# Optimization experiments

Measured on AMD Instinct MI355X. Metric: run time of the kernel, lower is better.

Reference implementation:

```python
import jax, jax.numpy as jnp
import numpy as np

EPS = 1e-12  # torch F.normalize eps

def _normalize(x):
    n = jnp.sqrt(jnp.sum(x * x, axis=-1, keepdims=True))
    return x / jnp.maximum(n, EPS)

def bgs_extended(d6s):
    # d6s: [B, N, D, 3, 2] -> rotation [B, N, D, 3, 3] (columns b1,b2,b3)
    b1 = _normalize(d6s[..., :, 0])
    a2 = d6s[..., :, 1]
    dot = jnp.sum(b1 * a2, axis=-1, keepdims=True)
    b2 = _normalize(a2 - dot * b1)
    b3 = jnp.cross(b1, b2, axis=-1)
    return jnp.stack([b1, b2, b3], axis=-1)

def setup_inputs() -> dict:
    key = jax.random.key(0)
    k1, k2, k3, k4, k5 = jax.random.split(key, 5)
    B, N, D, F = 8, 8192, 64, 64
    X = jax.random.normal(k1, (B, N, D, 3), dtype=jnp.float32)
    J = jax.random.normal(k2, (B, N, D, 3, 2), dtype=jnp.float32)
    A = jax.random.normal(k3, (F, D), dtype=jnp.float32)
    Bm = jax.random.normal(k4, (F, D), dtype=jnp.float32)
    C = jax.random.normal(k5, (F, D), dtype=jnp.float32)
    return {"X": X, "J": J, "A": A, "Bm": Bm, "C": C}

def reference(X, J, A, Bm, C):
    R = bgs_extended(J)  # [B,N,D,3,3]
    # RT_i X = dot(column i of R, X) -> compute all three at once: [B,N,D,3]
    RTX = jnp.einsum('bndki,bndk->bndi', R, X)
    rt0, rt1, rt2 = RTX[..., 0:1], RTX[..., 1:2], RTX[..., 2:3]
    # get_rrtx(i, R, s) == R[..., :, i] * s
    a_term = R[..., :, 0] * rt0 + R[..., :, 1] * rt1
    b_term = R[..., :, 1] * rt0 - R[..., :, 0] * rt1
    c_term = R[..., :, 2] * rt2
    Y = (jnp.einsum('fe,bnei->bnfi', A, a_term)
         + jnp.einsum('fe,bnei->bnfi', Bm, b_term)
         + jnp.einsum('fe,bnei->bnfi', C, c_term))
    return Y
```

## Files before the change

### kernel.cpp

```cpp
#include <hip/hip_runtime.h>

typedef __bf16 bf16;
typedef bf16 bf16x8 __attribute__((ext_vector_type(8)));
typedef float f32x4 __attribute__((ext_vector_type(4)));
typedef unsigned int u32;

#define PTS 16
#define WREG 4800

__device__ __forceinline__ void gld_lds16(const void* g, void* l) {
    __builtin_amdgcn_global_load_lds(
        (const __attribute__((address_space(1))) u32*)g,
        (__attribute__((address_space(3))) u32*)l, 16, 0, 0);
}

__global__ __launch_bounds__(256, 7)
void affine_linear_fused(const float* __restrict__ X, const float* __restrict__ J,
                         const float* __restrict__ A, const float* __restrict__ Bm,
                         const float* __restrict__ C, float* __restrict__ Y)
{
    __shared__ __attribute__((aligned(128))) unsigned char lds[4 * WREG];

    const int tid  = threadIdx.x;
    const int wave = tid >> 6;
    const int lane = tid & 63;
    const int l16  = lane & 15;
    const int lq   = lane >> 4;
    const long bn0 = (long)blockIdx.x * PTS;

    unsigned char* wbase = &lds[wave * WREG];

    const float* xg = X + (bn0 + wave * 4) * 192;
    #pragma unroll
    for (int t = 0; t < 3; ++t)
        gld_lds16(xg + t * 256 + lane * 4, wbase + t * 1024);

    const float* jg = J + (bn0 + wave * 4) * 384 + lane * 6;
    float jv[4][6];
    #pragma unroll
    for (int q = 0; q < 4; ++q) {
        float2 ja = *(const float2*)(jg + q * 384 + 0);
        float2 jb = *(const float2*)(jg + q * 384 + 2);
        float2 jc = *(const float2*)(jg + q * 384 + 4);
        jv[q][0] = ja.x; jv[q][1] = ja.y;
        jv[q][2] = jb.x; jv[q][3] = jb.y;
        jv[q][4] = jc.x; jv[q][5] = jc.y;
    }

    __asm__ volatile("s_waitcnt vmcnt(0)" ::: "memory");

    const float* xlds = (const float*)wbase;
    float xv[4][3];
    #pragma unroll
    for (int q = 0; q < 4; ++q) {
        const float* xp = xlds + q * 192 + lane * 3;
        xv[q][0] = xp[0]; xv[q][1] = xp[1]; xv[q][2] = xp[2];
    }

    #pragma unroll
    for (int q = 0; q < 4; ++q) {
        float a1x = jv[q][0], a2x = jv[q][1];
        float a1y = jv[q][2], a2y = jv[q][3];
        float a1z = jv[q][4], a2z = jv[q][5];
        float xx = xv[q][0], xy = xv[q][1], xz = xv[q][2];

        float n1sq = a1x*a1x + a1y*a1y + a1z*a1z;
        float inv1 = __builtin_amdgcn_rsqf(fmaxf(n1sq, 1e-24f));
        float b1x = a1x*inv1, b1y = a1y*inv1, b1z = a1z*inv1;
        float dot = b1x*a2x + b1y*a2y + b1z*a2z;
        float ux = a2x - dot*b1x, uy = a2y - dot*b1y, uz = a2z - dot*b1z;
        float n2sq = ux*ux + uy*uy + uz*uz;
        float inv2 = __builtin_amdgcn_rsqf(fmaxf(n2sq, 1e-24f));
        float b2x = ux*inv2, b2y = uy*inv2, b2z = uz*inv2;
        float b3x = b1y*b2z - b1z*b2y;
        float b3y = b1z*b2x - b1x*b2z;
        float b3z = b1x*b2y - b1y*b2x;

        float rt0 = b1x*xx + b1y*xy + b1z*xz;
        float rt1 = b2x*xx + b2y*xy + b2z*xz;
        float rt2 = b3x*xx + b3y*xy + b3z*xz;

        float at0 = b1x*rt0 + b2x*rt1;
        float at1 = b1y*rt0 + b2y*rt1;
        float at2 = b1z*rt0 + b2z*rt1;
        float bt0 = b2x*rt0 - b1x*rt1;
        float bt1 = b2y*rt0 - b1y*rt1;
        float bt2 = b2z*rt0 - b1z*rt1;
        float ct0 = b3x*rt2, ct1 = b3y*rt2, ct2 = b3z*rt2;

        bf16* r0 = (bf16*)(wbase + (q*3 + 0) * 400);
        bf16* r1 = (bf16*)(wbase + (q*3 + 1) * 400);
        bf16* r2 = (bf16*)(wbase + (q*3 + 2) * 400);
        r0[lane] = (bf16)at0; r0[64+lane] = (bf16)bt0; r0[128+lane] = (bf16)ct0;
        r1[lane] = (bf16)at1; r1[64+lane] = (bf16)bt1; r1[128+lane] = (bf16)ct1;
        r2[lane] = (bf16)at2; r2[64+lane] = (bf16)bt2; r2[128+lane] = (bf16)ct2;
    }

    const int f = wave * 16 + l16;
    const float* wp0 = A + f * 64 + lq * 8;
    f32x4 wlo = *(const f32x4*)wp0;
    f32x4 whi = *(const f32x4*)(wp0 + 4);

    __syncthreads();

    const unsigned char* arow[3];
    #pragma unroll
    for (int mt = 0; mt < 3; ++mt) {
        int m  = mt * 16 + l16;
        int wv = m / 12;
        int r  = m - wv * 12;
        arow[mt] = &lds[wv * WREG + r * 400] + lq * 16;
    }
    f32x4 acc[3];
    #pragma unroll
    for (int mt = 0; mt < 3; ++mt) acc[mt] = (f32x4){0.f, 0.f, 0.f, 0.f};

    #pragma unroll
    for (int kk = 0; kk < 6; ++kk) {
        f32x4 nlo = wlo, nhi = whi;
        if (kk < 5) {
            const float* src = (kk + 1 < 2) ? A : (kk + 1 < 4) ? Bm : C;
            const float* p = src + f * 64 + ((kk + 1) & 1) * 32 + lq * 8;
            nlo = *(const f32x4*)p;
            nhi = *(const f32x4*)(p + 4);
        }
        bf16x8 w;
        w[0] = (bf16)wlo[0]; w[1] = (bf16)wlo[1]; w[2] = (bf16)wlo[2]; w[3] = (bf16)wlo[3];
        w[4] = (bf16)whi[0]; w[5] = (bf16)whi[1]; w[6] = (bf16)whi[2]; w[7] = (bf16)whi[3];
        #pragma unroll
        for (int mt = 0; mt < 3; ++mt) {
            bf16x8 af = *(const bf16x8*)(arow[mt] + kk * 64);
            acc[mt] = __builtin_amdgcn_mfma_f32_16x16x32_bf16(af, w, acc[mt], 0, 0, 0);
        }
        wlo = nlo; whi = nhi;
    }

    __syncthreads();

    float* yw = (float*)wbase;
    #pragma unroll
    for (int mt = 0; mt < 3; ++mt) {
        #pragma unroll
        for (int r = 0; r < 4; ++r) {
            int m  = mt * 16 + lq * 4 + r;
            int wv = m / 12;
            int rr = m - wv * 12;
            int q  = rr / 3;
            int i  = rr - q * 3;
            int p  = wv * 4 + q;
            yw[p * 48 + l16 * 3 + i] = acc[mt][r];
        }
    }

    const f32x4* ysrc = (const f32x4*)yw;
    #pragma unroll
    for (int v = 0; v < 3; ++v) {
        int vi = v * 64 + lane;
        int p  = vi / 12;
        int vo = vi - p * 12;
        f32x4* dst = (f32x4*)(Y + (bn0 + p) * 192 + wave * 48) + vo;
        *dst = ysrc[vi];
    }
}

extern "C" void kernel_launch(void* const* d_in, const int* in_sizes, int n_in,
                              void* d_out, int out_size, void* d_ws, size_t ws_size,
                              hipStream_t stream) {
    const float* X  = (const float*)d_in[0];
    const float* J  = (const float*)d_in[1];
    const float* A  = (const float*)d_in[2];
    const float* Bm = (const float*)d_in[3];
    const float* C  = (const float*)d_in[4];
    float* Y = (float*)d_out;

    const int points = in_sizes[0] / (64 * 3);
    const int blocks = points / PTS;
    affine_linear_fused<<<blocks, 256, 0, stream>>>(X, J, A, Bm, C, Y);
}
```

Before: 206.9 us.

## Process four point groups per block with register prefetch and hoisted bf16 weights

```diff
diff --git a/kernel.cpp b/kernel.cpp
--- a/kernel.cpp
+++ b/kernel.cpp
@@ -3,18 +3,35 @@
 typedef __bf16 bf16;
 typedef bf16 bf16x8 __attribute__((ext_vector_type(8)));
 typedef float f32x4 __attribute__((ext_vector_type(4)));
-typedef unsigned int u32;
 
 #define PTS 16
+#define NG 4
 #define WREG 4800
 
-__device__ __forceinline__ void gld_lds16(const void* g, void* l) {
-    __builtin_amdgcn_global_load_lds(
-        (const __attribute__((address_space(1))) u32*)g,
-        (__attribute__((address_space(3))) u32*)l, 16, 0, 0);
+__device__ __forceinline__ void load_group(
+    const float* __restrict__ J, const float* __restrict__ X,
+    long bn0, int wave, int lane, float jv[4][6], float xv[4][3])
+{
+    const float* jg = J + (bn0 + wave * 4) * 384 + lane * 6;
+    #pragma unroll
+    for (int q = 0; q < 4; ++q) {
+        float2 ja = *(const float2*)(jg + q * 384 + 0);
+        float2 jb = *(const float2*)(jg + q * 384 + 2);
+        float2 jc2 = *(const float2*)(jg + q * 384 + 4);
+        jv[q][0] = ja.x; jv[q][1] = ja.y;
+        jv[q][2] = jb.x; jv[q][3] = jb.y;
+        jv[q][4] = jc2.x; jv[q][5] = jc2.y;
+    }
+    const float* xg = X + (bn0 + wave * 4) * 192 + lane * 3;
+    #pragma unroll
+    for (int q = 0; q < 4; ++q) {
+        xv[q][0] = xg[q * 192 + 0];
+        xv[q][1] = xg[q * 192 + 1];
+        xv[q][2] = xg[q * 192 + 2];
+    }
 }
 
-__global__ __launch_bounds__(256, 7)
+__global__ __launch_bounds__(256, 4)
 void affine_linear_fused(const float* __restrict__ X, const float* __restrict__ J,
                          const float* __restrict__ A, const float* __restrict__ Bm,
                          const float* __restrict__ C, float* __restrict__ Y)
@@ -26,82 +43,25 @@
     const int lane = tid & 63;
     const int l16  = lane & 15;
     const int lq   = lane >> 4;
-    const long bn0 = (long)blockIdx.x * PTS;
-
     unsigned char* wbase = &lds[wave * WREG];
 
-    const float* xg = X + (bn0 + wave * 4) * 192;
-    #pragma unroll
-    for (int t = 0; t < 3; ++t)
-        gld_lds16(xg + t * 256 + lane * 4, wbase + t * 1024);
+    const long gbase = (long)blockIdx.x * NG;
 
-    const float* jg = J + (bn0 + wave * 4) * 384 + lane * 6;
-    float jv[4][6];
-    #pragma unroll
-    for (int q = 0; q < 4; ++q) {
-        float2 ja = *(const float2*)(jg + q * 384 + 0);
-        float2 jb = *(const float2*)(jg + q * 384 + 2);
-        float2 jc = *(const float2*)(jg + q * 384 + 4);
-        jv[q][0] = ja.x; jv[q][1] = ja.y;
-        jv[q][2] = jb.x; jv[q][3] = jb.y;
-        jv[q][4] = jc.x; jv[q][5] = jc.y;
-    }
-
-    __asm__ volatile("s_waitcnt vmcnt(0)" ::: "memory");
-
-    const float* xlds = (const float*)wbase;
-    float xv[4][3];
-    #pragma unroll
-    for (int q = 0; q < 4; ++q) {
-        const float* xp = xlds + q * 192 + lane * 3;
-        xv[q][0] = xp[0]; xv[q][1] = xp[1]; xv[q][2] = xp[2];
-    }
-
-    #pragma unroll
-    for (int q = 0; q < 4; ++q) {
-        float a1x = jv[q][0], a2x = jv[q][1];
-        float a1y = jv[q][2], a2y = jv[q][3];
-        float a1z = jv[q][4], a2z = jv[q][5];
-        float xx = xv[q][0], xy = xv[q][1], xz = xv[q][2];
-
-        float n1sq = a1x*a1x + a1y*a1y + a1z*a1z;
-        float inv1 = __builtin_amdgcn_rsqf(fmaxf(n1sq, 1e-24f));
-        float b1x = a1x*inv1, b1y = a1y*inv1, b1z = a1z*inv1;
-        float dot = b1x*a2x + b1y*a2y + b1z*a2z;
-        float ux = a2x - dot*b1x, uy = a2y - dot*b1y, uz = a2z - dot*b1z;
-        float n2sq = ux*ux + uy*uy + uz*uz;
-        float inv2 = __builtin_amdgcn_rsqf(fmaxf(n2sq, 1e-24f));
-        float b2x = ux*inv2, b2y = uy*inv2, b2z = uz*inv2;
-        float b3x = b1y*b2z - b1z*b2y;
-        float b3y = b1z*b2x - b1x*b2z;
-        float b3z = b1x*b2y - b1y*b2x;
-
-        float rt0 = b1x*xx + b1y*xy + b1z*xz;
-        float rt1 = b2x*xx + b2y*xy + b2z*xz;
-        float rt2 = b3x*xx + b3y*xy + b3z*xz;
-
-        float at0 = b1x*rt0 + b2x*rt1;
-        float at1 = b1y*rt0 + b2y*rt1;
-        float at2 = b1z*rt0 + b2z*rt1;
-        float bt0 = b2x*rt0 - b1x*rt1;
-        float bt1 = b2y*rt0 - b1y*rt1;
-        float bt2 = b2z*rt0 - b1z*rt1;
-        float ct0 = b3x*rt2, ct1 = b3y*rt2, ct2 = b3z*rt2;
-
-        bf16* r0 = (bf16*)(wbase + (q*3 + 0) * 400);
-        bf16* r1 = (bf16*)(wbase + (q*3 + 1) * 400);
-        bf16* r2 = (bf16*)(wbase + (q*3 + 2) * 400);
-        r0[lane] = (bf16)at0; r0[64+lane] = (bf16)bt0; r0[128+lane] = (bf16)ct0;
-        r1[lane] = (bf16)at1; r1[64+lane] = (bf16)bt1; r1[128+lane] = (bf16)ct1;
-        r2[lane] = (bf16)at2; r2[64+lane] = (bf16)bt2; r2[128+lane] = (bf16)ct2;
-    }
+    float jc[4][6], xc[4][3];
+    load_group(J, X, gbase * PTS, wave, lane, jc, xc);
 
     const int f = wave * 16 + l16;
-    const float* wp0 = A + f * 64 + lq * 8;
-    f32x4 wlo = *(const f32x4*)wp0;
-    f32x4 whi = *(const f32x4*)(wp0 + 4);
-
-    __syncthreads();
+    bf16x8 wfrag[6];
+    #pragma unroll
+    for (int kk = 0; kk < 6; ++kk) {
+        const float* src = (kk < 2) ? A : (kk < 4) ? Bm : C;
+        const f32x4* p4 = (const f32x4*)(src + f * 64 + (kk & 1) * 32 + lq * 8);
+        f32x4 lo = p4[0], hi = p4[1];
+        bf16x8 w;
+        w[0] = (bf16)lo[0]; w[1] = (bf16)lo[1]; w[2] = (bf16)lo[2]; w[3] = (bf16)lo[3];
+        w[4] = (bf16)hi[0]; w[5] = (bf16)hi[1]; w[6] = (bf16)hi[2]; w[7] = (bf16)hi[3];
+        wfrag[kk] = w;
+    }
 
     const unsigned char* arow[3];
     #pragma unroll
@@ -111,55 +71,106 @@
         int r  = m - wv * 12;
         arow[mt] = &lds[wv * WREG + r * 400] + lq * 16;
     }
-    f32x4 acc[3];
-    #pragma unroll
-    for (int mt = 0; mt < 3; ++mt) acc[mt] = (f32x4){0.f, 0.f, 0.f, 0.f};
 
     #pragma unroll
-    for (int kk = 0; kk < 6; ++kk) {
-        f32x4 nlo = wlo, nhi = whi;
-        if (kk < 5) {
-            const float* src = (kk + 1 < 2) ? A : (kk + 1 < 4) ? Bm : C;
-            const float* p = src + f * 64 + ((kk + 1) & 1) * 32 + lq * 8;
-            nlo = *(const f32x4*)p;
-            nhi = *(const f32x4*)(p + 4);
+    for (int g = 0; g < NG; ++g) {
+        float jn[4][6], xn[4][3];
+        if (g + 1 < NG)
+            load_group(J, X, (gbase + g + 1) * PTS, wave, lane, jn, xn);
+
+        const long bn0 = (gbase + g) * PTS;
+
+        #pragma unroll
+        for (int q = 0; q < 4; ++q) {
+            float a1x = jc[q][0], a2x = jc[q][1];
+            float a1y = jc[q][2], a2y = jc[q][3];
+            float a1z = jc[q][4], a2z = jc[q][5];
+            float xx = xc[q][0], xy = xc[q][1], xz = xc[q][2];
+
+            float n1sq = a1x*a1x + a1y*a1y + a1z*a1z;
+            float inv1 = __builtin_amdgcn_rsqf(fmaxf(n1sq, 1e-24f));
+            float b1x = a1x*inv1, b1y = a1y*inv1, b1z = a1z*inv1;
+            float dot = b1x*a2x + b1y*a2y + b1z*a2z;
+            float ux = a2x - dot*b1x, uy = a2y - dot*b1y, uz = a2z - dot*b1z;
+            float n2sq = ux*ux + uy*uy + uz*uz;
+            float inv2 = __builtin_amdgcn_rsqf(fmaxf(n2sq, 1e-24f));
+            float b2x = ux*inv2, b2y = uy*inv2, b2z = uz*inv2;
+            float b3x = b1y*b2z - b1z*b2y;
+            float b3y = b1z*b2x - b1x*b2z;
+            float b3z = b1x*b2y - b1y*b2x;
+
+            float rt0 = b1x*xx + b1y*xy + b1z*xz;
+            float rt1 = b2x*xx + b2y*xy + b2z*xz;
+            float rt2 = b3x*xx + b3y*xy + b3z*xz;
+
+            float at0 = b1x*rt0 + b2x*rt1;
+            float at1 = b1y*rt0 + b2y*rt1;
+            float at2 = b1z*rt0 + b2z*rt1;
+            float bt0 = b2x*rt0 - b1x*rt1;
+            float bt1 = b2y*rt0 - b1y*rt1;
+            float bt2 = b2z*rt0 - b1z*rt1;
+            float ct0 = b3x*rt2, ct1 = b3y*rt2, ct2 = b3z*rt2;
+
+            bf16* r0 = (bf16*)(wbase + (q*3 + 0) * 400);
+            bf16* r1 = (bf16*)(wbase + (q*3 + 1) * 400);
+            bf16* r2 = (bf16*)(wbase + (q*3 + 2) * 400);
+            r0[lane] = (bf16)at0; r0[64+lane] = (bf16)bt0; r0[128+lane] = (bf16)ct0;
+            r1[lane] = (bf16)at1; r1[64+lane] = (bf16)bt1; r1[128+lane] = (bf16)ct1;
+            r2[lane] = (bf16)at2; r2[64+lane] = (bf16)bt2; r2[128+lane] = (bf16)ct2;
         }
-        bf16x8 w;
-        w[0] = (bf16)wlo[0]; w[1] = (bf16)wlo[1]; w[2] = (bf16)wlo[2]; w[3] = (bf16)wlo[3];
-        w[4] = (bf16)whi[0]; w[5] = (bf16)whi[1]; w[6] = (bf16)whi[2]; w[7] = (bf16)whi[3];
+
+        __asm__ volatile("s_waitcnt lgkmcnt(0)" ::: "memory");
+        __builtin_amdgcn_s_barrier();
+
+        f32x4 acc[3];
+        #pragma unroll
+        for (int mt = 0; mt < 3; ++mt) acc[mt] = (f32x4){0.f, 0.f, 0.f, 0.f};
+        #pragma unroll
+        for (int kk = 0; kk < 6; ++kk) {
+            #pragma unroll
+            for (int mt = 0; mt < 3; ++mt) {
+                bf16x8 af = *(const bf16x8*)(arow[mt] + kk * 64);
+                acc[mt] = __builtin_amdgcn_mfma_f32_16x16x32_bf16(af, wfrag[kk], acc[mt], 0, 0, 0);
+            }
+        }
+
+        __asm__ volatile("s_waitcnt lgkmcnt(0)" ::: "memory");
+        __builtin_amdgcn_s_barrier();
+
+        float* yw = (float*)wbase;
         #pragma unroll
         for (int mt = 0; mt < 3; ++mt) {
-            bf16x8 af = *(const bf16x8*)(arow[mt] + kk * 64);
-            acc[mt] = __builtin_amdgcn_mfma_f32_16x16x32_bf16(af, w, acc[mt], 0, 0, 0);
+            #pragma unroll
+            for (int r = 0; r < 4; ++r) {
+                int m  = mt * 16 + lq * 4 + r;
+                int wv = m / 12;
+                int rr = m - wv * 12;
+                int q  = rr / 3;
+                int i  = rr - q * 3;
+                int p  = wv * 4 + q;
+                yw[p * 48 + l16 * 3 + i] = acc[mt][r];
+            }
         }
-        wlo = nlo; whi = nhi;
-    }
 
-    __syncthreads();
+        const f32x4* ysrc = (const f32x4*)yw;
+        #pragma unroll
+        for (int v = 0; v < 3; ++v) {
+            int vi = v * 64 + lane;
+            int p  = vi / 12;
+            int vo = vi - p * 12;
+            f32x4* dst = (f32x4*)(Y + (bn0 + p) * 192 + wave * 48) + vo;
+            *dst = ysrc[vi];
+        }
 
-    float* yw = (float*)wbase;
-    #pragma unroll
-    for (int mt = 0; mt < 3; ++mt) {
-        #pragma unroll
-        for (int r = 0; r < 4; ++r) {
-            int m  = mt * 16 + lq * 4 + r;
-            int wv = m / 12;
-            int rr = m - wv * 12;
-            int q  = rr / 3;
-            int i  = rr - q * 3;
-            int p  = wv * 4 + q;
-            yw[p * 48 + l16 * 3 + i] = acc[mt][r];
+        if (g + 1 < NG) {
+            #pragma unroll
+            for (int q = 0; q < 4; ++q) {
+                #pragma unroll
+                for (int k = 0; k < 6; ++k) jc[q][k] = jn[q][k];
+                #pragma unroll
+                for (int k = 0; k < 3; ++k) xc[q][k] = xn[q][k];
+            }
         }
-    }
-
-    const f32x4* ysrc = (const f32x4*)yw;
-    #pragma unroll
-    for (int v = 0; v < 3; ++v) {
-        int vi = v * 64 + lane;
-        int p  = vi / 12;
-        int vo = vi - p * 12;
-        f32x4* dst = (f32x4*)(Y + (bn0 + p) * 192 + wave * 48) + vo;
-        *dst = ysrc[vi];
     }
 }
 
@@ -174,6 +185,6 @@
     float* Y = (float*)d_out;
 
     const int points = in_sizes[0] / (64 * 3);
-    const int blocks = points / PTS;
+    const int blocks = points / (PTS * NG);
     affine_linear_fused<<<blocks, 256, 0, stream>>>(X, J, A, Bm, C, Y);
 }
```

Measured after the change: 206.7 us. Within noise of the previous version (-0.1%).
